# Optimization experiments

Hardware: AMD Instinct MI355X
Metric: run time of the kernel (lower is better)

Reference implementation:

```python
import jax, jax.numpy as jnp
import numpy as np

B, D_IN, D_H = 4096, 1024, 1024  # cell_dim == hidden_dim required by the elementwise math


def _lin(x, W, b):
    # torch nn.Linear: y = x @ W.T + b, W: [out, in]
    return x @ W.T + b


def setup_inputs() -> dict:
    key = jax.random.key(0)
    ks = jax.random.split(key, 20)
    s2 = 1.0 / np.sqrt(D_IN + D_H)
    s1 = 1.0 / np.sqrt(D_IN)
    inp = {
        "input_tensor": jax.random.normal(ks[0], (B, D_IN), jnp.float32),
        "h_cur": jax.random.uniform(ks[1], (B, D_H), jnp.float32),
        "excited_cell": jax.random.uniform(ks[2], (B, D_H), jnp.float32),
        "time_cell": jax.random.uniform(ks[3], (B, D_H), jnp.float32),
        "Wt_w": jax.random.normal(ks[4], (D_H, D_IN + D_H), jnp.float32) * s2,
        "Wt_b": jax.random.normal(ks[5], (D_H,), jnp.float32) * s2,
        "Wa_w": jax.random.normal(ks[6], (D_H, D_IN + D_H), jnp.float32) * s2,
        "Wa_b": jax.random.normal(ks[7], (D_H,), jnp.float32) * s2,
        "Eh_w": jax.random.normal(ks[8], (D_H, D_IN + D_H), jnp.float32) * s2,
        "Eh_b": jax.random.normal(ks[9], (D_H,), jnp.float32) * s2,
        "Hw_w": jax.random.normal(ks[10], (D_H, D_IN + D_H), jnp.float32) * s2,
        "Hw_b": jax.random.normal(ks[11], (D_H,), jnp.float32) * s2,
        "Tr_w": jax.random.normal(ks[12], (D_H, D_IN), jnp.float32) * s1,
        "Tr_b": jax.random.normal(ks[13], (D_H,), jnp.float32) * s1,
        "Ei_w": jax.random.normal(ks[14], (D_H, D_IN), jnp.float32) * s1,
        "Ei_b": jax.random.normal(ks[15], (D_H,), jnp.float32) * s1,
    }
    return inp


def reference(input_tensor, h_cur, excited_cell, time_cell,
              Wt_w, Wt_b, Wa_w, Wa_b, Eh_w, Eh_b, Hw_w, Hw_b,
              Tr_w, Tr_b, Ei_w, Ei_b):
    combined = jnp.concatenate([input_tensor, h_cur], axis=1)  # [B, D_IN+D_H]
    energy_init = jax.nn.sigmoid(_lin(input_tensor, Ei_w, Ei_b))
    ratio = jax.nn.sigmoid(_lin(input_tensor, Tr_w, Tr_b))
    up_time = jnp.tanh(_lin(combined, Wt_w, Wt_b))
    time_cell = ratio * jax.nn.relu(time_cell + up_time) - 1.0
    leap = (time_cell <= 0).astype(jnp.float32)
    time_cell = (1.0 - leap) * time_cell
    energy = leap * excited_cell
    excited_cell = excited_cell - energy + energy_init * (1.0 - leap)
    absorb_energy = jax.nn.sigmoid(_lin(combined, Wa_w, Wa_b))
    excited_cell = excited_cell + absorb_energy
    h_up = h_cur * energy
    h_state = jnp.tanh(_lin(jnp.concatenate([input_tensor, h_up], axis=1), Eh_w, Eh_b))
    h_weight = jax.nn.sigmoid(_lin(combined, Hw_w, Hw_b))
    h_next = jnp.tanh((1.0 - h_weight) * h_cur + h_weight * h_state)
    return (h_next, excited_cell, time_cell)
```

## Files before the change

### kernel.cpp

```cpp
#include <hip/hip_runtime.h>
#include <math.h>


typedef __attribute__((ext_vector_type(4))) float f32x4;
typedef __attribute__((ext_vector_type(8))) _Float16 half8;
typedef __attribute__((ext_vector_type(4))) _Float16 half4;

#define NEL (4096 * 1024)

__device__ __forceinline__ float sigm(float x) { return 1.0f / (1.0f + expf(-x)); }

__device__ __forceinline__ void gload16(const void* g, void* l) {
  __builtin_amdgcn_global_load_lds(
      (const __attribute__((address_space(1))) void*)g,
      (__attribute__((address_space(3))) void*)l, 16, 0, 0);
}

template <int OP, bool SPLIT>
__device__ __forceinline__ void gemm_body(
    _Float16* sm,
    const _Float16* A1h, const _Float16* A1l,
    const _Float16* A2h, const _Float16* A2l,
    const _Float16* Wh,  const _Float16* Wl,
    const float* bias, const int K,
    float* outF, _Float16* outH, const float* hw_p, const float* hc_p)
{
  _Float16* AsH = sm;
  _Float16* BsH = sm + 4096;
  _Float16* AsL = sm + 8192;
  _Float16* BsL = sm + 12288;
  const int tid = threadIdx.x;
  const int lane = tid & 63;
  const int w = tid >> 6;
  const int wr = w >> 1, wc = w & 1;
  const int brow = blockIdx.x * 128;
  const int bcol = blockIdx.y * 128;
  const int lr = lane & 15, lq = lane >> 4;
  const int r0 = tid >> 2;
  const int cb = (tid & 3) * 8;

  f32x4 acc[4][4] = {};

  for (int k0 = 0; k0 < K; k0 += 32) {
    const _Float16* Ah = (k0 < 1024) ? A1h : A2h;
    const _Float16* Al = (k0 < 1024) ? A1l : A2l;
    const int kk = k0 & 1023;
    __syncthreads();
    {
      const size_t ao  = (size_t)(brow + r0) * 1024 + kk + cb;
      const size_t ao2 = (size_t)(brow + r0 + 64) * 1024 + kk + cb;
      const size_t bo  = (size_t)(bcol + r0) * K + k0 + cb;
      const size_t bo2 = (size_t)(bcol + r0 + 64) * K + k0 + cb;
      gload16(Ah + ao,  &AsH[r0 * 32 + cb]);
      gload16(Ah + ao2, &AsH[(r0 + 64) * 32 + cb]);
      gload16(Wh + bo,  &BsH[r0 * 32 + cb]);
      gload16(Wh + bo2, &BsH[(r0 + 64) * 32 + cb]);
      if (SPLIT) {
        gload16(Al + ao,  &AsL[r0 * 32 + cb]);
        gload16(Al + ao2, &AsL[(r0 + 64) * 32 + cb]);
        gload16(Wl + bo,  &BsL[r0 * 32 + cb]);
        gload16(Wl + bo2, &BsL[(r0 + 64) * 32 + cb]);
      }
    }
    __syncthreads();

    half8 ah[4], bh[4], al[4], bl[4];
#pragma unroll
    for (int m = 0; m < 4; ++m) {
      const int row = wr * 64 + m * 16 + lr;
      ah[m] = *(const half8*)&AsH[row * 32 + lq * 8];
      if (SPLIT) al[m] = *(const half8*)&AsL[row * 32 + lq * 8];
    }
#pragma unroll
    for (int n = 0; n < 4; ++n) {
      const int row = wc * 64 + n * 16 + lr;
      bh[n] = *(const half8*)&BsH[row * 32 + lq * 8];
      if (SPLIT) bl[n] = *(const half8*)&BsL[row * 32 + lq * 8];
    }
#pragma unroll
    for (int m = 0; m < 4; ++m)
#pragma unroll
      for (int n = 0; n < 4; ++n) {
        acc[m][n] = __builtin_amdgcn_mfma_f32_16x16x32_f16(ah[m], bh[n], acc[m][n], 0, 0, 0);
        if (SPLIT) {
          acc[m][n] = __builtin_amdgcn_mfma_f32_16x16x32_f16(ah[m], bl[n], acc[m][n], 0, 0, 0);
          acc[m][n] = __builtin_amdgcn_mfma_f32_16x16x32_f16(al[m], bh[n], acc[m][n], 0, 0, 0);
        }
      }
  }

  float bv[4];
#pragma unroll
  for (int n = 0; n < 4; ++n) bv[n] = bias[bcol + wc * 64 + n * 16 + lr];

#pragma unroll
  for (int m = 0; m < 4; ++m)
#pragma unroll
    for (int n = 0; n < 4; ++n) {
      const int col = bcol + wc * 64 + n * 16 + lr;
#pragma unroll
      for (int j = 0; j < 4; ++j) {
        const int rowg = brow + wr * 64 + m * 16 + lq * 4 + j;
        const size_t idx = (size_t)rowg * 1024 + col;
        const float v = acc[m][n][j] + bv[n];
        if (OP == 0)      outF[idx] = sigm(v);
        else if (OP == 1) outF[idx] = tanhf(v);
        else if (OP == 2) outH[idx] = (_Float16)sigm(v);
        else {
          const float hs = tanhf(v);
          const float hwv = hw_p[idx];
          const float hcv = hc_p[idx];
          outF[idx] = tanhf((1.0f - hwv) * hcv + hwv * hs);
        }
      }
    }
}

__global__ __launch_bounds__(256, 2)
void qurnn_gemm5(const _Float16* inpH, const _Float16* inpL,
                 const _Float16* hcH,  const _Float16* hcL,
                 const _Float16* WtH, const _Float16* WtL, const float* Wt_b,
                 const _Float16* TrH, const _Float16* TrL, const float* Tr_b,
                 const _Float16* WaH, const float* Wa_b,
                 const _Float16* HwH, const float* Hw_b,
                 const _Float16* EiH, const float* Ei_b,
                 float* ws_ut, float* out_tm, float* out_ex, float* out_h,
                 _Float16* ws_ei)
{
  __shared__ __align__(16) _Float16 sm[4 * 4096];
  switch (blockIdx.z) {
    case 0: gemm_body<1, true >(sm, inpH, inpL, hcH, hcL, WtH, WtL, Wt_b, 2048, ws_ut,  nullptr, nullptr, nullptr); break;
    case 1: gemm_body<0, true >(sm, inpH, inpL, nullptr, nullptr, TrH, TrL, Tr_b, 1024, out_tm, nullptr, nullptr, nullptr); break;
    case 2: gemm_body<0, false>(sm, inpH, nullptr, hcH, nullptr, WaH, nullptr, Wa_b, 2048, out_ex, nullptr, nullptr, nullptr); break;
    case 3: gemm_body<0, false>(sm, inpH, nullptr, hcH, nullptr, HwH, nullptr, Hw_b, 2048, out_h,  nullptr, nullptr, nullptr); break;
    default:gemm_body<2, false>(sm, inpH, nullptr, nullptr, nullptr, EiH, nullptr, Ei_b, 1024, nullptr, ws_ei, nullptr, nullptr); break;
  }
}

__global__ __launch_bounds__(256, 2)
void qurnn_eh(const _Float16* inpH, const _Float16* hup,
              const _Float16* EhH, const float* Eh_b,
              const float* hcur, float* out_h)
{
  __shared__ __align__(16) _Float16 sm[2 * 4096];
  gemm_body<3, false>(sm, inpH, nullptr, hup, nullptr, EhH, nullptr, Eh_b, 2048,
                      out_h, nullptr, out_h, hcur);
}

__global__ __launch_bounds__(256)
void qurnn_cell(const f32x4* tc, const f32x4* ec, const f32x4* hc,
                const f32x4* ut, const half4* ei,
                f32x4* out_ex, f32x4* out_tm, half4* hup)
{
  const int i = blockIdx.x * 256 + threadIdx.x;
  const f32x4 tcv = tc[i], ecv = ec[i], hcv = hc[i];
  const f32x4 rav = out_tm[i];
  const f32x4 utv = ut[i];
  const f32x4 abv = out_ex[i];
  const half4 eiv = ei[i];
  f32x4 to, eo; half4 ho;
#pragma unroll
  for (int j = 0; j < 4; ++j) {
    const float t = rav[j] * fmaxf(tcv[j] + utv[j], 0.0f) - 1.0f;
    const bool leap = (t <= 0.0f);
    to[j] = leap ? 0.0f : t;
    eo[j] = (leap ? 0.0f : ecv[j] + (float)eiv[j]) + abv[j];
    ho[j] = (_Float16)(leap ? hcv[j] * ecv[j] : 0.0f);
  }
  out_tm[i] = to;
  out_ex[i] = eo;
  hup[i] = ho;
}

__global__ __launch_bounds__(256)
void convert_k(const float* inp, const float* hcur,
               const float* Wt_w, const float* Tr_w, const float* Wa_w,
               const float* Hw_w, const float* Eh_w, const float* Ei_w,
               _Float16* inpH, _Float16* inpL, _Float16* hcH, _Float16* hcL,
               _Float16* WtH, _Float16* WtL, _Float16* TrH, _Float16* TrL,
               _Float16* WaH, _Float16* HwH, _Float16* EhH, _Float16* EiH)
{
  const float* src; _Float16* dh; _Float16* dl; int n4;
  switch (blockIdx.z) {
    case 0: src = inp;  dh = inpH; dl = inpL; n4 = NEL / 4;     break;
    case 1: src = hcur; dh = hcH;  dl = hcL;  n4 = NEL / 4;     break;
    case 2: src = Wt_w; dh = WtH;  dl = WtL;  n4 = (1024*2048)/4; break;
    case 3: src = Tr_w; dh = TrH;  dl = TrL;  n4 = (1024*1024)/4; break;
    case 4: src = Wa_w; dh = WaH;  dl = nullptr; n4 = (1024*2048)/4; break;
    case 5: src = Hw_w; dh = HwH;  dl = nullptr; n4 = (1024*2048)/4; break;
    case 6: src = Eh_w; dh = EhH;  dl = nullptr; n4 = (1024*2048)/4; break;
    default:src = Ei_w; dh = EiH;  dl = nullptr; n4 = (1024*1024)/4; break;
  }
  for (int i = blockIdx.x * 256 + threadIdx.x; i < n4; i += gridDim.x * 256) {
    const f32x4 v = ((const f32x4*)src)[i];
    half4 h, l;
#pragma unroll
    for (int j = 0; j < 4; ++j) {
      h[j] = (_Float16)v[j];
      l[j] = (_Float16)(v[j] - (float)h[j]);
    }
    ((half4*)dh)[i] = h;
    if (dl) ((half4*)dl)[i] = l;
  }
}

extern "C" void kernel_launch(void* const* d_in, const int* in_sizes, int n_in,
                              void* d_out, int out_size, void* d_ws, size_t ws_size,
                              hipStream_t stream)
{
  const float* inp  = (const float*)d_in[0];
  const float* hcur = (const float*)d_in[1];
  const float* ec   = (const float*)d_in[2];
  const float* tc   = (const float*)d_in[3];
  const float* Wt_w = (const float*)d_in[4];
  const float* Wt_b = (const float*)d_in[5];
  const float* Wa_w = (const float*)d_in[6];
  const float* Wa_b = (const float*)d_in[7];
  const float* Eh_w = (const float*)d_in[8];
  const float* Eh_b = (const float*)d_in[9];
  const float* Hw_w = (const float*)d_in[10];
  const float* Hw_b = (const float*)d_in[11];
  const float* Tr_w = (const float*)d_in[12];
  const float* Tr_b = (const float*)d_in[13];
  const float* Ei_w = (const float*)d_in[14];
  const float* Ei_b = (const float*)d_in[15];

  float* out_h  = (float*)d_out;
  float* out_ex = out_h + NEL;
  float* out_tm = out_ex + NEL;

  char* wsb = (char*)d_ws;
  float*    ws_ut  = (float*)(wsb);
  _Float16* ws_hup = (_Float16*)(wsb + (16u << 20));
  _Float16* ws_ei  = (_Float16*)(wsb + (24u << 20));
  _Float16* inpH   = (_Float16*)(wsb + (32u << 20));
  _Float16* inpL   = (_Float16*)(wsb + (40u << 20));
  _Float16* hcH    = (_Float16*)(wsb + (48u << 20));
  _Float16* hcL    = (_Float16*)(wsb + (56u << 20));
  _Float16* WtH    = (_Float16*)(wsb + (64u << 20));
  _Float16* WtL    = (_Float16*)(wsb + (68u << 20));
  _Float16* TrH    = (_Float16*)(wsb + (72u << 20));
  _Float16* TrL    = (_Float16*)(wsb + (74u << 20));
  _Float16* WaH    = (_Float16*)(wsb + (76u << 20));
  _Float16* HwH    = (_Float16*)(wsb + (80u << 20));
  _Float16* EhH    = (_Float16*)(wsb + (84u << 20));
  _Float16* EiH    = (_Float16*)(wsb + (88u << 20));

  convert_k<<<dim3(512, 1, 8), 256, 0, stream>>>(
      inp, hcur, Wt_w, Tr_w, Wa_w, Hw_w, Eh_w, Ei_w,
      inpH, inpL, hcH, hcL, WtH, WtL, TrH, TrL, WaH, HwH, EhH, EiH);

  qurnn_gemm5<<<dim3(32, 8, 5), 256, 0, stream>>>(
      inpH, inpL, hcH, hcL, WtH, WtL, Wt_b, TrH, TrL, Tr_b,
      WaH, Wa_b, HwH, Hw_b, EiH, Ei_b,
      ws_ut, out_tm, out_ex, out_h, ws_ei);

  qurnn_cell<<<dim3(4096), 256, 0, stream>>>(
      (const f32x4*)tc, (const f32x4*)ec, (const f32x4*)hcur,
      (const f32x4*)ws_ut, (const half4*)ws_ei,
      (f32x4*)out_ex, (f32x4*)out_tm, (half4*)ws_hup);

  qurnn_eh<<<dim3(32, 8), 256, 0, stream>>>(inpH, ws_hup, EhH, Eh_b, hcur, out_h);
}
```

Baseline: 233.1 us.

## Drop split-fp16 GEMMs, add exact fp32 fixup for near-threshold leap elements

Removes the hi/lo fp16 split (three MFMAs per tile) from the time-ratio and up-time GEMMs so every GEMM uses a single fp16 pass. Elements whose leap test value falls within a small band of zero are collected through an atomic list and recomputed in fp32 by a new fixup kernel, which protects the discontinuous leap decision. It also stores the sigmoid outputs as fp16 intermediates, halves LDS use to allow 3 blocks per CU, and adds a block-index swizzle for L2 reuse. The risks are the atomic contention, a capped list that may overflow, and reduced precision in non-leap outputs.

```diff
diff --git a/kernel.cpp b/kernel.cpp
--- a/kernel.cpp
+++ b/kernel.cpp
@@ -7,6 +7,8 @@
 typedef __attribute__((ext_vector_type(4))) _Float16 half4;
 
 #define NEL (4096 * 1024)
+#define DELTA 0.02f
+#define CAP 1300000
 
 __device__ __forceinline__ float sigm(float x) { return 1.0f / (1.0f + expf(-x)); }
 
@@ -16,25 +18,19 @@
       (__attribute__((address_space(3))) void*)l, 16, 0, 0);
 }
 
-template <int OP, bool SPLIT>
+template <int OP>
 __device__ __forceinline__ void gemm_body(
-    _Float16* sm,
-    const _Float16* A1h, const _Float16* A1l,
-    const _Float16* A2h, const _Float16* A2l,
-    const _Float16* Wh,  const _Float16* Wl,
-    const float* bias, const int K,
+    _Float16* sm, const int brow, const int bcol,
+    const _Float16* A1h, const _Float16* A2h,
+    const _Float16* Wh, const float* bias, const int K,
     float* outF, _Float16* outH, const float* hw_p, const float* hc_p)
 {
-  _Float16* AsH = sm;
-  _Float16* BsH = sm + 4096;
-  _Float16* AsL = sm + 8192;
-  _Float16* BsL = sm + 12288;
+  _Float16* As = sm;
+  _Float16* Bs = sm + 4096;
   const int tid = threadIdx.x;
   const int lane = tid & 63;
   const int w = tid >> 6;
   const int wr = w >> 1, wc = w & 1;
-  const int brow = blockIdx.x * 128;
-  const int bcol = blockIdx.y * 128;
   const int lr = lane & 15, lq = lane >> 4;
   const int r0 = tid >> 2;
   const int cb = (tid & 3) * 8;
@@ -43,50 +39,26 @@
 
   for (int k0 = 0; k0 < K; k0 += 32) {
     const _Float16* Ah = (k0 < 1024) ? A1h : A2h;
-    const _Float16* Al = (k0 < 1024) ? A1l : A2l;
     const int kk = k0 & 1023;
     __syncthreads();
-    {
-      const size_t ao  = (size_t)(brow + r0) * 1024 + kk + cb;
-      const size_t ao2 = (size_t)(brow + r0 + 64) * 1024 + kk + cb;
-      const size_t bo  = (size_t)(bcol + r0) * K + k0 + cb;
-      const size_t bo2 = (size_t)(bcol + r0 + 64) * K + k0 + cb;
-      gload16(Ah + ao,  &AsH[r0 * 32 + cb]);
-      gload16(Ah + ao2, &AsH[(r0 + 64) * 32 + cb]);
-      gload16(Wh + bo,  &BsH[r0 * 32 + cb]);
-      gload16(Wh + bo2, &BsH[(r0 + 64) * 32 + cb]);
-      if (SPLIT) {
-        gload16(Al + ao,  &AsL[r0 * 32 + cb]);
-        gload16(Al + ao2, &AsL[(r0 + 64) * 32 + cb]);
-        gload16(Wl + bo,  &BsL[r0 * 32 + cb]);
-        gload16(Wl + bo2, &BsL[(r0 + 64) * 32 + cb]);
-      }
-    }
+    gload16(Ah + (size_t)(brow + r0) * 1024 + kk + cb,      &As[r0 * 32 + cb]);
+    gload16(Ah + (size_t)(brow + r0 + 64) * 1024 + kk + cb, &As[(r0 + 64) * 32 + cb]);
+    gload16(Wh + (size_t)(bcol + r0) * K + k0 + cb,         &Bs[r0 * 32 + cb]);
+    gload16(Wh + (size_t)(bcol + r0 + 64) * K + k0 + cb,    &Bs[(r0 + 64) * 32 + cb]);
     __syncthreads();
 
-    half8 ah[4], bh[4], al[4], bl[4];
-#pragma unroll
-    for (int m = 0; m < 4; ++m) {
-      const int row = wr * 64 + m * 16 + lr;
-      ah[m] = *(const half8*)&AsH[row * 32 + lq * 8];
-      if (SPLIT) al[m] = *(const half8*)&AsL[row * 32 + lq * 8];
-    }
-#pragma unroll
-    for (int n = 0; n < 4; ++n) {
-      const int row = wc * 64 + n * 16 + lr;
-      bh[n] = *(const half8*)&BsH[row * 32 + lq * 8];
-      if (SPLIT) bl[n] = *(const half8*)&BsL[row * 32 + lq * 8];
-    }
+    half8 a[4], b[4];
 #pragma unroll
     for (int m = 0; m < 4; ++m)
-#pragma unroll
-      for (int n = 0; n < 4; ++n) {
-        acc[m][n] = __builtin_amdgcn_mfma_f32_16x16x32_f16(ah[m], bh[n], acc[m][n], 0, 0, 0);
-        if (SPLIT) {
-          acc[m][n] = __builtin_amdgcn_mfma_f32_16x16x32_f16(ah[m], bl[n], acc[m][n], 0, 0, 0);
-          acc[m][n] = __builtin_amdgcn_mfma_f32_16x16x32_f16(al[m], bh[n], acc[m][n], 0, 0, 0);
-        }
-      }
+      a[m] = *(const half8*)&As[(wr * 64 + m * 16 + lr) * 32 + lq * 8];
+#pragma unroll
+    for (int n = 0; n < 4; ++n)
+      b[n] = *(const half8*)&Bs[(wc * 64 + n * 16 + lr) * 32 + lq * 8];
+#pragma unroll
+    for (int m = 0; m < 4; ++m)
+#pragma unroll
+      for (int n = 0; n < 4; ++n)
+        acc[m][n] = __builtin_amdgcn_mfma_f32_16x16x32_f16(a[m], b[n], acc[m][n], 0, 0, 0);
   }
 
   float bv[4];
@@ -116,91 +88,142 @@
     }
 }
 
-__global__ __launch_bounds__(256, 2)
-void qurnn_gemm5(const _Float16* inpH, const _Float16* inpL,
-                 const _Float16* hcH,  const _Float16* hcL,
-                 const _Float16* WtH, const _Float16* WtL, const float* Wt_b,
-                 const _Float16* TrH, const _Float16* TrL, const float* Tr_b,
+__device__ __forceinline__ void swz_block(int id, int& bx, int& by) {
+  const int swz = (id & 7) * 32 + (id >> 3);
+  bx = swz & 31;
+  by = swz >> 5;
+}
+
+__global__ __launch_bounds__(256, 3)
+void qurnn_gemm5(const _Float16* inpH, const _Float16* hcH,
+                 const _Float16* WtH, const float* Wt_b,
                  const _Float16* WaH, const float* Wa_b,
                  const _Float16* HwH, const float* Hw_b,
+                 const _Float16* TrH, const float* Tr_b,
                  const _Float16* EiH, const float* Ei_b,
-                 float* ws_ut, float* out_tm, float* out_ex, float* out_h,
-                 _Float16* ws_ei)
-{
-  __shared__ __align__(16) _Float16 sm[4 * 4096];
+                 float* ws_ut, _Float16* ws_ab, float* out_h,
+                 _Float16* ws_ra, _Float16* ws_ei)
+{
+  __shared__ __align__(16) _Float16 sm[2 * 4096];
+  int bx, by; swz_block(blockIdx.x, bx, by);
+  const int brow = bx * 128, bcol = by * 128;
   switch (blockIdx.z) {
-    case 0: gemm_body<1, true >(sm, inpH, inpL, hcH, hcL, WtH, WtL, Wt_b, 2048, ws_ut,  nullptr, nullptr, nullptr); break;
-    case 1: gemm_body<0, true >(sm, inpH, inpL, nullptr, nullptr, TrH, TrL, Tr_b, 1024, out_tm, nullptr, nullptr, nullptr); break;
-    case 2: gemm_body<0, false>(sm, inpH, nullptr, hcH, nullptr, WaH, nullptr, Wa_b, 2048, out_ex, nullptr, nullptr, nullptr); break;
-    case 3: gemm_body<0, false>(sm, inpH, nullptr, hcH, nullptr, HwH, nullptr, Hw_b, 2048, out_h,  nullptr, nullptr, nullptr); break;
-    default:gemm_body<2, false>(sm, inpH, nullptr, nullptr, nullptr, EiH, nullptr, Ei_b, 1024, nullptr, ws_ei, nullptr, nullptr); break;
-  }
-}
-
-__global__ __launch_bounds__(256, 2)
+    case 0: gemm_body<1>(sm, brow, bcol, inpH, hcH, WtH, Wt_b, 2048, ws_ut, nullptr, nullptr, nullptr); break;
+    case 1: gemm_body<2>(sm, brow, bcol, inpH, hcH, WaH, Wa_b, 2048, nullptr, ws_ab, nullptr, nullptr); break;
+    case 2: gemm_body<0>(sm, brow, bcol, inpH, hcH, HwH, Hw_b, 2048, out_h, nullptr, nullptr, nullptr); break;
+    case 3: gemm_body<2>(sm, brow, bcol, inpH, nullptr, TrH, Tr_b, 1024, nullptr, ws_ra, nullptr, nullptr); break;
+    default:gemm_body<2>(sm, brow, bcol, inpH, nullptr, EiH, Ei_b, 1024, nullptr, ws_ei, nullptr, nullptr); break;
+  }
+}
+
+__global__ __launch_bounds__(256, 3)
 void qurnn_eh(const _Float16* inpH, const _Float16* hup,
               const _Float16* EhH, const float* Eh_b,
               const float* hcur, float* out_h)
 {
   __shared__ __align__(16) _Float16 sm[2 * 4096];
-  gemm_body<3, false>(sm, inpH, nullptr, hup, nullptr, EhH, nullptr, Eh_b, 2048,
-                      out_h, nullptr, out_h, hcur);
+  int bx, by; swz_block(blockIdx.x, bx, by);
+  gemm_body<3>(sm, bx * 128, by * 128, inpH, hup, EhH, Eh_b, 2048,
+               out_h, nullptr, out_h, hcur);
 }
 
 __global__ __launch_bounds__(256)
 void qurnn_cell(const f32x4* tc, const f32x4* ec, const f32x4* hc,
-                const f32x4* ut, const half4* ei,
-                f32x4* out_ex, f32x4* out_tm, half4* hup)
+                const f32x4* ut, const half4* ra, const half4* ab,
+                const half4* ei, f32x4* out_ex, f32x4* out_tm, half4* hup,
+                int* count, int* list)
 {
   const int i = blockIdx.x * 256 + threadIdx.x;
-  const f32x4 tcv = tc[i], ecv = ec[i], hcv = hc[i];
-  const f32x4 rav = out_tm[i];
-  const f32x4 utv = ut[i];
-  const f32x4 abv = out_ex[i];
-  const half4 eiv = ei[i];
+  const f32x4 tcv = tc[i], ecv = ec[i], hcv = hc[i], utv = ut[i];
+  const half4 rav = ra[i], abv = ab[i], eiv = ei[i];
   f32x4 to, eo; half4 ho;
 #pragma unroll
   for (int j = 0; j < 4; ++j) {
-    const float t = rav[j] * fmaxf(tcv[j] + utv[j], 0.0f) - 1.0f;
+    const float t = (float)rav[j] * fmaxf(tcv[j] + utv[j], 0.0f) - 1.0f;
     const bool leap = (t <= 0.0f);
     to[j] = leap ? 0.0f : t;
-    eo[j] = (leap ? 0.0f : ecv[j] + (float)eiv[j]) + abv[j];
+    eo[j] = (leap ? 0.0f : ecv[j] + (float)eiv[j]) + (float)abv[j];
     ho[j] = (_Float16)(leap ? hcv[j] * ecv[j] : 0.0f);
+    if (fabsf(t) < DELTA) {
+      const int pos = atomicAdd(count, 1);
+      if (pos < CAP) list[pos] = i * 4 + j;
+    }
   }
   out_tm[i] = to;
   out_ex[i] = eo;
   hup[i] = ho;
+}
+
+__global__ __launch_bounds__(256)
+void qurnn_fixup(const int* count, const int* list,
+                 const float* inp, const float* hcur,
+                 const float* Tr_w, const float* Tr_b,
+                 const float* Wt_w, const float* Wt_b,
+                 const _Float16* ei, const _Float16* ab,
+                 const float* tc, const float* ec,
+                 float* out_tm, float* out_ex, _Float16* hup)
+{
+  const int gtid = blockIdx.x * 256 + threadIdx.x;
+  const int wid = gtid >> 6, lane = gtid & 63;
+  const int nw = gridDim.x * 4;
+  const int n = min(*count, CAP);
+  for (int e = wid; e < n; e += nw) {
+    const int idx = list[e];
+    const int row = idx >> 10, col = idx & 1023;
+    float dTr = 0.0f, dWt = 0.0f;
+    const float* irow = inp + (size_t)row * 1024;
+    const float* hrow = hcur + (size_t)row * 1024;
+    const float* trw = Tr_w + (size_t)col * 1024;
+    const float* wtw = Wt_w + (size_t)col * 2048;
+    for (int k = lane; k < 1024; k += 64) {
+      const float a = irow[k];
+      dTr = fmaf(a, trw[k], dTr);
+      dWt = fmaf(a, wtw[k], dWt);
+      dWt = fmaf(hrow[k], wtw[1024 + k], dWt);
+    }
+#pragma unroll
+    for (int s = 32; s; s >>= 1) {
+      dTr += __shfl_down(dTr, s);
+      dWt += __shfl_down(dWt, s);
+    }
+    if (lane == 0) {
+      const float ratio = sigm(dTr + Tr_b[col]);
+      const float utv = tanhf(dWt + Wt_b[col]);
+      const float t = ratio * fmaxf(tc[idx] + utv, 0.0f) - 1.0f;
+      const bool leap = (t <= 0.0f);
+      out_tm[idx] = leap ? 0.0f : t;
+      out_ex[idx] = (leap ? 0.0f : ec[idx] + (float)ei[idx]) + (float)ab[idx];
+      hup[idx] = (_Float16)(leap ? hcur[idx] * ec[idx] : 0.0f);
+    }
+  }
 }
 
 __global__ __launch_bounds__(256)
 void convert_k(const float* inp, const float* hcur,
                const float* Wt_w, const float* Tr_w, const float* Wa_w,
                const float* Hw_w, const float* Eh_w, const float* Ei_w,
-               _Float16* inpH, _Float16* inpL, _Float16* hcH, _Float16* hcL,
-               _Float16* WtH, _Float16* WtL, _Float16* TrH, _Float16* TrL,
-               _Float16* WaH, _Float16* HwH, _Float16* EhH, _Float16* EiH)
-{
-  const float* src; _Float16* dh; _Float16* dl; int n4;
+               _Float16* inpH, _Float16* hcH, _Float16* WtH, _Float16* TrH,
+               _Float16* WaH, _Float16* HwH, _Float16* EhH, _Float16* EiH,
+               int* count)
+{
+  if (blockIdx.z == 0 && blockIdx.x == 0 && threadIdx.x == 0) *count = 0;
+  const float* src; _Float16* dh; int n4;
   switch (blockIdx.z) {
-    case 0: src = inp;  dh = inpH; dl = inpL; n4 = NEL / 4;     break;
-    case 1: src = hcur; dh = hcH;  dl = hcL;  n4 = NEL / 4;     break;
-    case 2: src = Wt_w; dh = WtH;  dl = WtL;  n4 = (1024*2048)/4; break;
-    case 3: src = Tr_w; dh = TrH;  dl = TrL;  n4 = (1024*1024)/4; break;
-    case 4: src = Wa_w; dh = WaH;  dl = nullptr; n4 = (1024*2048)/4; break;
-    case 5: src = Hw_w; dh = HwH;  dl = nullptr; n4 = (1024*2048)/4; break;
-    case 6: src = Eh_w; dh = EhH;  dl = nullptr; n4 = (1024*2048)/4; break;
-    default:src = Ei_w; dh = EiH;  dl = nullptr; n4 = (1024*1024)/4; break;
+    case 0: src = inp;  dh = inpH; n4 = NEL / 4;           break;
+    case 1: src = hcur; dh = hcH;  n4 = NEL / 4;           break;
+    case 2: src = Wt_w; dh = WtH;  n4 = (1024 * 2048) / 4; break;
+    case 3: src = Tr_w; dh = TrH;  n4 = (1024 * 1024) / 4; break;
+    case 4: src = Wa_w; dh = WaH;  n4 = (1024 * 2048) / 4; break;
+    case 5: src = Hw_w; dh = HwH;  n4 = (1024 * 2048) / 4; break;
+    case 6: src = Eh_w; dh = EhH;  n4 = (1024 * 2048) / 4; break;
+    default:src = Ei_w; dh = EiH;  n4 = (1024 * 1024) / 4; break;
   }
   for (int i = blockIdx.x * 256 + threadIdx.x; i < n4; i += gridDim.x * 256) {
     const f32x4 v = ((const f32x4*)src)[i];
-    half4 h, l;
-#pragma unroll
-    for (int j = 0; j < 4; ++j) {
-      h[j] = (_Float16)v[j];
-      l[j] = (_Float16)(v[j] - (float)h[j]);
-    }
+    half4 h;
+#pragma unroll
+    for (int j = 0; j < 4; ++j) h[j] = (_Float16)v[j];
     ((half4*)dh)[i] = h;
-    if (dl) ((half4*)dl)[i] = l;
   }
 }
 
@@ -231,34 +254,38 @@
 
   char* wsb = (char*)d_ws;
   float*    ws_ut  = (float*)(wsb);
-  _Float16* ws_hup = (_Float16*)(wsb + (16u << 20));
-  _Float16* ws_ei  = (_Float16*)(wsb + (24u << 20));
-  _Float16* inpH   = (_Float16*)(wsb + (32u << 20));
-  _Float16* inpL   = (_Float16*)(wsb + (40u << 20));
-  _Float16* hcH    = (_Float16*)(wsb + (48u << 20));
-  _Float16* hcL    = (_Float16*)(wsb + (56u << 20));
+  _Float16* ws_ra  = (_Float16*)(wsb + (16u << 20));
+  _Float16* ws_ab  = (_Float16*)(wsb + (24u << 20));
+  _Float16* ws_ei  = (_Float16*)(wsb + (32u << 20));
+  _Float16* ws_hup = (_Float16*)(wsb + (40u << 20));
+  _Float16* inpH   = (_Float16*)(wsb + (48u << 20));
+  _Float16* hcH    = (_Float16*)(wsb + (56u << 20));
   _Float16* WtH    = (_Float16*)(wsb + (64u << 20));
-  _Float16* WtL    = (_Float16*)(wsb + (68u << 20));
-  _Float16* TrH    = (_Float16*)(wsb + (72u << 20));
-  _Float16* TrL    = (_Float16*)(wsb + (74u << 20));
-  _Float16* WaH    = (_Float16*)(wsb + (76u << 20));
-  _Float16* HwH    = (_Float16*)(wsb + (80u << 20));
-  _Float16* EhH    = (_Float16*)(wsb + (84u << 20));
-  _Float16* EiH    = (_Float16*)(wsb + (88u << 20));
+  _Float16* TrH    = (_Float16*)(wsb + (68u << 20));
+  _Float16* WaH    = (_Float16*)(wsb + (70u << 20));
+  _Float16* HwH    = (_Float16*)(wsb + (74u << 20));
+  _Float16* EhH    = (_Float16*)(wsb + (78u << 20));
+  _Float16* EiH    = (_Float16*)(wsb + (82u << 20));
+  int*      d_cnt  = (int*)(wsb + (84u << 20));
+  int*      d_list = (int*)(wsb + (84u << 20) + 256);
 
   convert_k<<<dim3(512, 1, 8), 256, 0, stream>>>(
       inp, hcur, Wt_w, Tr_w, Wa_w, Hw_w, Eh_w, Ei_w,
-      inpH, inpL, hcH, hcL, WtH, WtL, TrH, TrL, WaH, HwH, EhH, EiH);
-
-  qurnn_gemm5<<<dim3(32, 8, 5), 256, 0, stream>>>(
-      inpH, inpL, hcH, hcL, WtH, WtL, Wt_b, TrH, TrL, Tr_b,
-      WaH, Wa_b, HwH, Hw_b, EiH, Ei_b,
-      ws_ut, out_tm, out_ex, out_h, ws_ei);
+      inpH, hcH, WtH, TrH, WaH, HwH, EhH, EiH, d_cnt);
+
+  qurnn_gemm5<<<dim3(256, 1, 5), 256, 0, stream>>>(
+      inpH, hcH, WtH, Wt_b, WaH, Wa_b, HwH, Hw_b, TrH, Tr_b, EiH, Ei_b,
+      ws_ut, ws_ab, out_h, ws_ra, ws_ei);
 
   qurnn_cell<<<dim3(4096), 256, 0, stream>>>(
       (const f32x4*)tc, (const f32x4*)ec, (const f32x4*)hcur,
-      (const f32x4*)ws_ut, (const half4*)ws_ei,
-      (f32x4*)out_ex, (f32x4*)out_tm, (half4*)ws_hup);
-
-  qurnn_eh<<<dim3(32, 8), 256, 0, stream>>>(inpH, ws_hup, EhH, Eh_b, hcur, out_h);
-}
+      (const f32x4*)ws_ut, (const half4*)ws_ra, (const half4*)ws_ab,
+      (const half4*)ws_ei, (f32x4*)out_ex, (f32x4*)out_tm, (half4*)ws_hup,
+      d_cnt, d_list);
+
+  qurnn_fixup<<<dim3(512), 256, 0, stream>>>(
+      d_cnt, d_list, inp, hcur, Tr_w, Tr_b, Wt_w, Wt_b,
+      ws_ei, ws_ab, tc, ec, out_tm, out_ex, ws_hup);
+
+  qurnn_eh<<<dim3(256), 256, 0, stream>>>(inpH, ws_hup, EhH, Eh_b, hcur, out_h);
+}
```

After: 545.1 us. 2.34x slower.
